# Optimization experiments

Measured on AMD Instinct MI355X. Metric: run time of the kernel, lower is better.

The kernel has to match this reference:

```python
import jax, jax.numpy as jnp
import numpy as np
from jax import lax

B, S, E = 8, 2048, 1024
NH, K = 4, 4
DH = E // NH  # 256


def setup_inputs() -> dict:
    key = jax.random.key(0)
    ks = jax.random.split(key, 8)
    sc = 0.02  # small_init-style scale
    return {
        "x": jax.random.normal(ks[0], (B, S, E), jnp.float32),
        "conv_w": jax.random.normal(ks[1], (K, 1, E), jnp.float32) * sc,  # depthwise (W,1,E)
        "conv_b": jnp.zeros((E,), jnp.float32),
        "fgate_w": jax.random.normal(ks[2], (NH, DH, DH), jnp.float32) * sc,
        "igate_w": jax.random.normal(ks[3], (NH, DH, DH), jnp.float32) * sc,
        "zgate_w": jax.random.normal(ks[4], (NH, DH, DH), jnp.float32) * sc,
        "ogate_w": jax.random.normal(ks[5], (NH, DH, DH), jnp.float32) * sc,
        "rkernel": jax.random.normal(ks[6], (NH, DH, 4 * DH), jnp.float32) * sc,
        "rbias": jnp.zeros((NH, 4, DH), jnp.float32),
        "gn_weight": jnp.ones((E,), jnp.float32),
    }


def _headwise(x, w):
    # LinearHeadwiseExpand, bias=False: einsum('...hd,hod->...ho')
    Bx, Sx, _ = x.shape
    return jnp.einsum('bshd,hod->bsho', x.reshape(Bx, Sx, NH, DH), w)


def reference(x, conv_w, conv_b, fgate_w, igate_w, zgate_w, ogate_w, rkernel, rbias, gn_weight):
    # --- causal depthwise conv1d + SiLU ---
    xp = jnp.pad(x, ((0, 0), (K - 1, 0), (0, 0)))  # left pad -> causal
    xc = lax.conv_general_dilated(
        xp, conv_w, window_strides=(1,), padding='VALID',
        dimension_numbers=('NWC', 'WIO', 'NWC'), feature_group_count=E) + conv_b
    x_conv = xc * jax.nn.sigmoid(xc)  # SiLU

    # --- headwise gate pre-activations (matches torch cat order [i,f,z,o]) ---
    gi = _headwise(x_conv, fgate_w)
    gf = _headwise(x_conv, igate_w)
    gz = _headwise(x, zgate_w)
    go = _headwise(x, ogate_w)
    gx = jnp.stack([gi, gf, gz, go], axis=3)      # (B,S,NH,4,DH)
    gx_t = jnp.moveaxis(gx, 1, 0)                 # (S,B,NH,4,DH)

    # --- stabilized exponential-gated sLSTM recurrence (xLSTM vanilla cell) ---
    z0 = jnp.zeros((B, NH, DH), x.dtype)

    def step(carry, xt):
        y, c, n, m = carry  # each (B,NH,DH)
        ry = jnp.einsum('bhd,hdk->bhk', y, rkernel).reshape(B, NH, 4, DH)
        raw = xt + ry + rbias
        ir, fr, zr, orr = raw[:, :, 0], raw[:, :, 1], raw[:, :, 2], raw[:, :, 3]
        logfplusm = m + jax.nn.log_sigmoid(fr)
        mnew = jnp.maximum(ir, logfplusm)
        ig = jnp.exp(ir - mnew)
        fg = jnp.exp(logfplusm - mnew)
        cnew = fg * c + ig * jnp.tanh(zr)
        nnew = fg * n + ig
        ynew = jax.nn.sigmoid(orr) * cnew / nnew
        return (ynew, cnew, nnew, mnew), ynew

    _, ys = lax.scan(step, (z0, z0, z0, z0), gx_t)  # ys: (S,B,NH,DH)
    y = jnp.moveaxis(ys, 0, 1)                       # (B,S,NH,DH)

    # --- MultiHeadLayerNorm: group_norm with num_groups=NH, weight only (no bias) ---
    mu = jnp.mean(y, axis=-1, keepdims=True)
    var = jnp.var(y, axis=-1, keepdims=True)
    yn = (y - mu) * lax.rsqrt(var + 1e-5)
    out = (yn * gn_weight.reshape(NH, DH)).reshape(B, S, E)
    return out
```

## Files before the change

kernel.cpp:

```cpp
#include <hip/hip_runtime.h>
#include <hip/hip_fp16.h>

#define BB 8
#define SS 2048
#define EE 1024
#define NHH 4
#define DHH 256

typedef _Float16 f16x2 __attribute__((ext_vector_type(2)));
typedef _Float16 f16x8 __attribute__((ext_vector_type(8)));
typedef float f32x4 __attribute__((ext_vector_type(4)));

__device__ __forceinline__ __half2 u2h2(unsigned int u) {
  union { unsigned int u; __half2 h; } c; c.u = u; return c.h;
}
__device__ __forceinline__ unsigned int h2u(__half2 h) {
  union { unsigned int u; __half2 h; } c; c.h = h; return c.u;
}

__global__ __launch_bounds__(256) void gates_gemm(
    const float* __restrict__ x, const float* __restrict__ conv_w,
    const float* __restrict__ conv_b,
    const float* __restrict__ fgw, const float* __restrict__ igw,
    const float* __restrict__ zgw, const float* __restrict__ ogw,
    __half* __restrict__ gx)
{
  __shared__ float Xs[8][11][33];
  __shared__ __half As[64][40];
  __shared__ __half Bs[64][40];

  const int tid = threadIdx.x;
  const int mt = blockIdx.x;
  const int nt = blockIdx.y;
  const int p  = blockIdx.z;
  const int h  = p >> 1, pair = p & 1;
  const int s0 = mt << 3;
  const int n0 = nt << 6;

  const float* W0 = pair ? zgw : fgw;
  const float* W1 = pair ? ogw : igw;

  const int w = tid >> 6, l = tid & 63;
  const int lrow = l & 15, kq = l >> 4;
  const int koff = kq << 3;

  f32x4 acc[4] = {};

  for (int d0 = 0; d0 < DHH; d0 += 32) {
    const int ebase = h * DHH + d0;

    if (pair == 0) {
      for (int i = tid; i < 8 * 11 * 32; i += 256) {
        int kk = i & 31, rest = i >> 5;
        int b = rest / 11, si = rest - b * 11;
        int sg = s0 - 3 + si;
        float v = 0.f;
        if (sg >= 0) v = x[((size_t)b * SS + sg) * EE + ebase + kk];
        Xs[b][si][kk] = v;
      }
      __syncthreads();
      for (int i = tid; i < 64 * 32; i += 256) {
        int kk = i & 31, r = i >> 5;
        int sl = r >> 3, b = r & 7;
        int e = ebase + kk;
        float xc = conv_b[e];
        xc = fmaf(Xs[b][sl + 0][kk], conv_w[0 * EE + e], xc);
        xc = fmaf(Xs[b][sl + 1][kk], conv_w[1 * EE + e], xc);
        xc = fmaf(Xs[b][sl + 2][kk], conv_w[2 * EE + e], xc);
        xc = fmaf(Xs[b][sl + 3][kk], conv_w[3 * EE + e], xc);
        float sg = 1.f / (1.f + __expf(-xc));
        As[r][kk] = __float2half(xc * sg);
      }
    } else {
      for (int i = tid; i < 64 * 32; i += 256) {
        int kk = i & 31, r = i >> 5;
        int sl = r >> 3, b = r & 7;
        As[r][kk] = __float2half(x[((size_t)b * SS + s0 + sl) * EE + ebase + kk]);
      }
    }
    for (int i = tid; i < 64 * 32; i += 256) {
      int k = i & 31, col = i >> 5;
      int o = n0 + col;
      const float* Wp = (o < 256) ? W0 : W1;
      int oo = o & 255;
      Bs[col][k] = __float2half(Wp[((size_t)h * DHH + oo) * DHH + d0 + k]);
    }
    __syncthreads();

    f16x8 bfrag = *(const f16x8*)&Bs[w * 16 + lrow][koff];
#pragma unroll
    for (int mtl = 0; mtl < 4; ++mtl) {
      f16x8 afrag = *(const f16x8*)&As[mtl * 16 + lrow][koff];
      acc[mtl] = __builtin_amdgcn_mfma_f32_16x16x32_f16(afrag, bfrag, acc[mtl], 0, 0, 0);
    }
    __syncthreads();
  }

#pragma unroll
  for (int mtl = 0; mtl < 4; ++mtl) {
#pragma unroll
    for (int j = 0; j < 4; ++j) {
      int row_loc = mtl * 16 + kq * 4 + j;
      int grow = s0 * 8 + row_loc;
      int colg = n0 + w * 16 + lrow;
      gx[(size_t)grow * 4096 + h * 1024 + pair * 512 + colg] = __float2half(acc[mtl][j]);
    }
  }
}

__global__ __launch_bounds__(512)
void slstm_scan4(
    const float* __restrict__ rk,
    const float* __restrict__ rb,
    const __half* __restrict__ gx,
    float* __restrict__ out)
{
  extern __shared__ unsigned char smem[];
  uint4* ldsB  = (uint4*)smem;
  __half* ypub = (__half*)(smem + 131072);
  float* rawb  = (float*)(smem + 132096);

  const int t = threadIdx.x;
  const int w = t >> 6, l = t & 63;
  const int lrow = l & 15, lkq = l >> 4;
  const int b = blockIdx.x >> 2, h = blockIdx.x & 3;
  const float* Rh = rk + (size_t)h * DHH * 1024;
  const int n0w = w << 7;

  f16x8 wB[6][8];
#pragma unroll
  for (int nt = 0; nt < 6; ++nt) {
    const int col = n0w + nt * 16 + lrow;
#pragma unroll
    for (int kt = 0; kt < 8; ++kt) {
      f16x8 f;
#pragma unroll
      for (int i = 0; i < 4; ++i) {
        const int k = kt * 32 + lkq * 8 + 2 * i;
        f[2 * i]     = (_Float16)Rh[(size_t)k * 1024 + col];
        f[2 * i + 1] = (_Float16)Rh[(size_t)(k + 1) * 1024 + col];
      }
      wB[nt][kt] = f;
    }
  }
  for (int j = 0; j < 2; ++j) {
    const int col = n0w + (6 + j) * 16 + lrow;
    for (int kt = 0; kt < 8; ++kt) {
      f16x8 f;
      for (int i = 0; i < 4; ++i) {
        const int k = kt * 32 + lkq * 8 + 2 * i;
        f[2 * i]     = (_Float16)Rh[(size_t)k * 1024 + col];
        f[2 * i + 1] = (_Float16)Rh[(size_t)(k + 1) * 1024 + col];
      }
      *(f16x8*)&ldsB[((w * 2 + j) * 8 + kt) * 64 + l] = f;
    }
  }

  const int d = t & 255;
  float rb0 = 0.f, rb1 = 0.f, rb2 = 0.f, rb3 = 0.f;
  if (t < 256) {
    rb0 = rb[h * 1024 + d];
    rb1 = rb[h * 1024 + 256 + d];
    rb2 = rb[h * 1024 + 512 + d];
    rb3 = rb[h * 1024 + 768 + d];
    ypub[d] = __float2half(0.f);
    ypub[256 + d] = __float2half(0.f);
  }
  __syncthreads();

  float cst = 0.f, nst = 0.f, mst = 0.f;
  const size_t gxstep = (size_t)BB * NHH * 1024;
  const __half* gp = gx + ((size_t)b * NHH + h) * 1024;
  float cx0 = 0.f, cx1 = 0.f, cx2 = 0.f, cx3 = 0.f;
  if (t < 256) {
    cx0 = __half2float(gp[d]);
    cx1 = __half2float(gp[256 + d]);
    cx2 = __half2float(gp[512 + d]);
    cx3 = __half2float(gp[768 + d]);
  }

  int cur = 0;
  for (int st = 0; st < SS; ++st) {
    __half nx0, nx1, nx2, nx3;
    if (t < 256) {
      const __half* pn = gp + (size_t)((st + 1 < SS) ? st + 1 : st) * gxstep;
      nx0 = pn[d]; nx1 = pn[256 + d]; nx2 = pn[512 + d]; nx3 = pn[768 + d];
    }

    const __half* yc = ypub + cur * 256;
    f32x4 a0 = {}, a1 = {}, a2 = {}, a3 = {}, a4 = {}, a5 = {}, a6 = {}, a7 = {};
#pragma unroll
    for (int kt = 0; kt < 8; ++kt) {
      f16x8 A = {};
      if (lrow == 0) A = *(const f16x8*)(yc + kt * 32 + lkq * 8);
      a0 = __builtin_amdgcn_mfma_f32_16x16x32_f16(A, wB[0][kt], a0, 0, 0, 0);
      a1 = __builtin_amdgcn_mfma_f32_16x16x32_f16(A, wB[1][kt], a1, 0, 0, 0);
      a2 = __builtin_amdgcn_mfma_f32_16x16x32_f16(A, wB[2][kt], a2, 0, 0, 0);
      a3 = __builtin_amdgcn_mfma_f32_16x16x32_f16(A, wB[3][kt], a3, 0, 0, 0);
      a4 = __builtin_amdgcn_mfma_f32_16x16x32_f16(A, wB[4][kt], a4, 0, 0, 0);
      a5 = __builtin_amdgcn_mfma_f32_16x16x32_f16(A, wB[5][kt], a5, 0, 0, 0);
      f16x8 b6 = *(const f16x8*)&ldsB[((w * 2 + 0) * 8 + kt) * 64 + l];
      f16x8 b7 = *(const f16x8*)&ldsB[((w * 2 + 1) * 8 + kt) * 64 + l];
      a6 = __builtin_amdgcn_mfma_f32_16x16x32_f16(A, b6, a6, 0, 0, 0);
      a7 = __builtin_amdgcn_mfma_f32_16x16x32_f16(A, b7, a7, 0, 0, 0);
    }
    if (l < 16) {
      rawb[n0w +   0 + l] = a0[0];
      rawb[n0w +  16 + l] = a1[0];
      rawb[n0w +  32 + l] = a2[0];
      rawb[n0w +  48 + l] = a3[0];
      rawb[n0w +  64 + l] = a4[0];
      rawb[n0w +  80 + l] = a5[0];
      rawb[n0w +  96 + l] = a6[0];
      rawb[n0w + 112 + l] = a7[0];
    }
    __syncthreads();

    if (t < 256) {
      float iv = rawb[d]       + cx0 + rb0;
      float fv = rawb[256 + d] + cx1 + rb1;
      float zv = rawb[512 + d] + cx2 + rb2;
      float ov = rawb[768 + d] + cx3 + rb3;

      float ea = __expf(-fabsf(fv));
      float ls = fminf(fv, 0.f) - __logf(1.f + ea);
      float lfm = mst + ls;
      float mn = fmaxf(iv, lfm);
      float ig = __expf(iv - mn);
      float fg = __expf(lfm - mn);
      float pz = __expf(-2.f * fabsf(zv));
      float tm = __fdividef(1.f - pz, 1.f + pz);
      float th = (zv < 0.f) ? -tm : tm;
      cst = fg * cst + ig * th;
      nst = fg * nst + ig;
      float og = __fdividef(1.f, 1.f + __expf(-ov));
      float y = og * __fdividef(cst, nst);
      mst = mn;

      out[((size_t)b * SS + st) * EE + h * DHH + d] = y;
      ypub[(cur ^ 1) * 256 + d] = __float2half(y);
    }
    __syncthreads();
    cur ^= 1;
    cx0 = __half2float(nx0); cx1 = __half2float(nx1);
    cx2 = __half2float(nx2); cx3 = __half2float(nx3);
  }
}

__global__ __launch_bounds__(256) void groupnorm(
    float* __restrict__ y, const float* __restrict__ gnw)
{
  const int row = blockIdx.x;
  const int t = threadIdx.x;
  float4 v = ((const float4*)y)[(size_t)row * 256 + t];
  float s = v.x + v.y + v.z + v.w;
  float q = v.x * v.x + v.y * v.y + v.z * v.z + v.w * v.w;
#pragma unroll
  for (int mask = 1; mask < 64; mask <<= 1) {
    s += __shfl_xor(s, mask, 64);
    q += __shfl_xor(q, mask, 64);
  }
  float mu = s * (1.f / 256.f);
  float var = q * (1.f / 256.f) - mu * mu;
  float rs = rsqrtf(var + 1e-5f);
  float4 g = ((const float4*)gnw)[t];
  float4 o;
  o.x = (v.x - mu) * rs * g.x;
  o.y = (v.y - mu) * rs * g.y;
  o.z = (v.z - mu) * rs * g.z;
  o.w = (v.w - mu) * rs * g.w;
  ((float4*)y)[(size_t)row * 256 + t] = o;
}

extern "C" void kernel_launch(void* const* d_in, const int* in_sizes, int n_in,
                              void* d_out, int out_size, void* d_ws, size_t ws_size,
                              hipStream_t stream) {
  const float* x      = (const float*)d_in[0];
  const float* conv_w = (const float*)d_in[1];
  const float* conv_b = (const float*)d_in[2];
  const float* fgw    = (const float*)d_in[3];
  const float* igw    = (const float*)d_in[4];
  const float* zgw    = (const float*)d_in[5];
  const float* ogw    = (const float*)d_in[6];
  const float* rk     = (const float*)d_in[7];
  const float* rb     = (const float*)d_in[8];
  const float* gnw    = (const float*)d_in[9];
  float* out = (float*)d_out;
  __half* gx = (__half*)d_ws;

  dim3 g1(256, 8, 8);
  gates_gemm<<<g1, 256, 0, stream>>>(x, conv_w, conv_b, fgw, igw, zgw, ogw, gx);

  const int scan_lds = 131072 + 1024 + 4096;
  (void)hipFuncSetAttribute(reinterpret_cast<const void*>(slstm_scan4),
                            hipFuncAttributeMaxDynamicSharedMemorySize, scan_lds);
  slstm_scan4<<<32, 512, scan_lds, stream>>>(rk, rb, gx, out);

  groupnorm<<<BB * SS, 256, 0, stream>>>(out, gnw);
}
```

Baseline: 4.348 ms.

## Keep more recurrent weights in registers and deepen gate prefetch in sLSTM scan

The scan kernel now holds 7 of 8 recurrent-weight column tiles per wave in registers instead of 6, which halves the LDS-resident weights and the per-step LDS reads. It preloads all A fragments and LDS B fragments before issuing the MFMAs, splits the MFMA chain into two groups of four accumulators, prefetches gate inputs two steps ahead instead of one, and replaces __syncthreads with an explicit lgkmcnt wait plus s_barrier. The aim is to shorten the serial per-timestep latency. The cost is higher register pressure, which risks spills. All lanes now load A instead of only lrow==0, which adds LDS traffic and may change results if the other rows were meant to be zero.

```diff
diff --git a/kernel.cpp b/kernel.cpp
--- a/kernel.cpp
+++ b/kernel.cpp
@@ -109,7 +109,7 @@
 }
 
 __global__ __launch_bounds__(512)
-void slstm_scan4(
+void slstm_scan5(
     const float* __restrict__ rk,
     const float* __restrict__ rb,
     const __half* __restrict__ gx,
@@ -117,8 +117,8 @@
 {
   extern __shared__ unsigned char smem[];
   uint4* ldsB  = (uint4*)smem;
-  __half* ypub = (__half*)(smem + 131072);
-  float* rawb  = (float*)(smem + 132096);
+  __half* ypub = (__half*)(smem + 65536);
+  float* rawb  = (float*)(smem + 66560);
 
   const int t = threadIdx.x;
   const int w = t >> 6, l = t & 63;
@@ -127,9 +127,9 @@
   const float* Rh = rk + (size_t)h * DHH * 1024;
   const int n0w = w << 7;
 
-  f16x8 wB[6][8];
-#pragma unroll
-  for (int nt = 0; nt < 6; ++nt) {
+  f16x8 wB[7][8];
+#pragma unroll
+  for (int nt = 0; nt < 7; ++nt) {
     const int col = n0w + nt * 16 + lrow;
 #pragma unroll
     for (int kt = 0; kt < 8; ++kt) {
@@ -143,8 +143,8 @@
       wB[nt][kt] = f;
     }
   }
-  for (int j = 0; j < 2; ++j) {
-    const int col = n0w + (6 + j) * 16 + lrow;
+  {
+    const int col = n0w + 112 + lrow;
     for (int kt = 0; kt < 8; ++kt) {
       f16x8 f;
       for (int i = 0; i < 4; ++i) {
@@ -152,7 +152,7 @@
         f[2 * i]     = (_Float16)Rh[(size_t)k * 1024 + col];
         f[2 * i + 1] = (_Float16)Rh[(size_t)(k + 1) * 1024 + col];
       }
-      *(f16x8*)&ldsB[((w * 2 + j) * 8 + kt) * 64 + l] = f;
+      *(f16x8*)&ldsB[(w * 8 + kt) * 64 + l] = f;
     }
   }
 
@@ -172,49 +172,70 @@
   const size_t gxstep = (size_t)BB * NHH * 1024;
   const __half* gp = gx + ((size_t)b * NHH + h) * 1024;
   float cx0 = 0.f, cx1 = 0.f, cx2 = 0.f, cx3 = 0.f;
+  __half nh0 = __float2half(0.f), nh1 = nh0, nh2 = nh0, nh3 = nh0;
   if (t < 256) {
     cx0 = __half2float(gp[d]);
     cx1 = __half2float(gp[256 + d]);
     cx2 = __half2float(gp[512 + d]);
     cx3 = __half2float(gp[768 + d]);
+    const __half* p1 = gp + gxstep;
+    nh0 = p1[d]; nh1 = p1[256 + d]; nh2 = p1[512 + d]; nh3 = p1[768 + d];
   }
 
   int cur = 0;
   for (int st = 0; st < SS; ++st) {
-    __half nx0, nx1, nx2, nx3;
+    __half p0 = nh0, p1 = nh1, p2 = nh2, p3 = nh3;
     if (t < 256) {
-      const __half* pn = gp + (size_t)((st + 1 < SS) ? st + 1 : st) * gxstep;
-      nx0 = pn[d]; nx1 = pn[256 + d]; nx2 = pn[512 + d]; nx3 = pn[768 + d];
+      const int sp = (st + 2 < SS) ? st + 2 : SS - 1;
+      const __half* pp = gp + (size_t)sp * gxstep;
+      p0 = pp[d]; p1 = pp[256 + d]; p2 = pp[512 + d]; p3 = pp[768 + d];
     }
 
     const __half* yc = ypub + cur * 256;
-    f32x4 a0 = {}, a1 = {}, a2 = {}, a3 = {}, a4 = {}, a5 = {}, a6 = {}, a7 = {};
-#pragma unroll
-    for (int kt = 0; kt < 8; ++kt) {
-      f16x8 A = {};
-      if (lrow == 0) A = *(const f16x8*)(yc + kt * 32 + lkq * 8);
-      a0 = __builtin_amdgcn_mfma_f32_16x16x32_f16(A, wB[0][kt], a0, 0, 0, 0);
-      a1 = __builtin_amdgcn_mfma_f32_16x16x32_f16(A, wB[1][kt], a1, 0, 0, 0);
-      a2 = __builtin_amdgcn_mfma_f32_16x16x32_f16(A, wB[2][kt], a2, 0, 0, 0);
-      a3 = __builtin_amdgcn_mfma_f32_16x16x32_f16(A, wB[3][kt], a3, 0, 0, 0);
-      a4 = __builtin_amdgcn_mfma_f32_16x16x32_f16(A, wB[4][kt], a4, 0, 0, 0);
-      a5 = __builtin_amdgcn_mfma_f32_16x16x32_f16(A, wB[5][kt], a5, 0, 0, 0);
-      f16x8 b6 = *(const f16x8*)&ldsB[((w * 2 + 0) * 8 + kt) * 64 + l];
-      f16x8 b7 = *(const f16x8*)&ldsB[((w * 2 + 1) * 8 + kt) * 64 + l];
-      a6 = __builtin_amdgcn_mfma_f32_16x16x32_f16(A, b6, a6, 0, 0, 0);
-      a7 = __builtin_amdgcn_mfma_f32_16x16x32_f16(A, b7, a7, 0, 0, 0);
-    }
-    if (l < 16) {
-      rawb[n0w +   0 + l] = a0[0];
-      rawb[n0w +  16 + l] = a1[0];
-      rawb[n0w +  32 + l] = a2[0];
-      rawb[n0w +  48 + l] = a3[0];
-      rawb[n0w +  64 + l] = a4[0];
-      rawb[n0w +  80 + l] = a5[0];
-      rawb[n0w +  96 + l] = a6[0];
-      rawb[n0w + 112 + l] = a7[0];
-    }
-    __syncthreads();
+    f16x8 Areg[8];
+#pragma unroll
+    for (int kt = 0; kt < 8; ++kt)
+      Areg[kt] = *(const f16x8*)(yc + kt * 32 + lkq * 8);
+    f16x8 b7[8];
+#pragma unroll
+    for (int kt = 0; kt < 8; ++kt)
+      b7[kt] = *(const f16x8*)&ldsB[(w * 8 + kt) * 64 + l];
+
+    {
+      f32x4 a0 = {}, a1 = {}, a2 = {}, a3 = {};
+#pragma unroll
+      for (int kt = 0; kt < 8; ++kt) {
+        a0 = __builtin_amdgcn_mfma_f32_16x16x32_f16(Areg[kt], wB[0][kt], a0, 0, 0, 0);
+        a1 = __builtin_amdgcn_mfma_f32_16x16x32_f16(Areg[kt], wB[1][kt], a1, 0, 0, 0);
+        a2 = __builtin_amdgcn_mfma_f32_16x16x32_f16(Areg[kt], wB[2][kt], a2, 0, 0, 0);
+        a3 = __builtin_amdgcn_mfma_f32_16x16x32_f16(Areg[kt], wB[3][kt], a3, 0, 0, 0);
+      }
+      if (l < 16) {
+        rawb[n0w +  0 + l] = a0[0];
+        rawb[n0w + 16 + l] = a1[0];
+        rawb[n0w + 32 + l] = a2[0];
+        rawb[n0w + 48 + l] = a3[0];
+      }
+    }
+    {
+      f32x4 c0 = {}, c1 = {}, c2 = {}, c3 = {};
+#pragma unroll
+      for (int kt = 0; kt < 8; ++kt) {
+        c0 = __builtin_amdgcn_mfma_f32_16x16x32_f16(Areg[kt], wB[4][kt], c0, 0, 0, 0);
+        c1 = __builtin_amdgcn_mfma_f32_16x16x32_f16(Areg[kt], wB[5][kt], c1, 0, 0, 0);
+        c2 = __builtin_amdgcn_mfma_f32_16x16x32_f16(Areg[kt], wB[6][kt], c2, 0, 0, 0);
+        c3 = __builtin_amdgcn_mfma_f32_16x16x32_f16(Areg[kt], b7[kt],    c3, 0, 0, 0);
+      }
+      if (l < 16) {
+        rawb[n0w +  64 + l] = c0[0];
+        rawb[n0w +  80 + l] = c1[0];
+        rawb[n0w +  96 + l] = c2[0];
+        rawb[n0w + 112 + l] = c3[0];
+      }
+    }
+
+    asm volatile("s_waitcnt lgkmcnt(0)" ::: "memory");
+    __builtin_amdgcn_s_barrier();
 
     if (t < 256) {
       float iv = rawb[d]       + cx0 + rb0;
@@ -240,10 +261,14 @@
       out[((size_t)b * SS + st) * EE + h * DHH + d] = y;
       ypub[(cur ^ 1) * 256 + d] = __float2half(y);
     }
-    __syncthreads();
+
+    asm volatile("s_waitcnt lgkmcnt(0)" ::: "memory");
+    __builtin_amdgcn_s_barrier();
+
     cur ^= 1;
-    cx0 = __half2float(nx0); cx1 = __half2float(nx1);
-    cx2 = __half2float(nx2); cx3 = __half2float(nx3);
+    cx0 = __half2float(nh0); cx1 = __half2float(nh1);
+    cx2 = __half2float(nh2); cx3 = __half2float(nh3);
+    nh0 = p0; nh1 = p1; nh2 = p2; nh3 = p3;
   }
 }
 
@@ -291,10 +316,10 @@
   dim3 g1(256, 8, 8);
   gates_gemm<<<g1, 256, 0, stream>>>(x, conv_w, conv_b, fgw, igw, zgw, ogw, gx);
 
-  const int scan_lds = 131072 + 1024 + 4096;
-  (void)hipFuncSetAttribute(reinterpret_cast<const void*>(slstm_scan4),
+  const int scan_lds = 65536 + 1024 + 4096;
+  (void)hipFuncSetAttribute(reinterpret_cast<const void*>(slstm_scan5),
                             hipFuncAttributeMaxDynamicSharedMemorySize, scan_lds);
-  slstm_scan4<<<32, 512, scan_lds, stream>>>(rk, rb, gx, out);
+  slstm_scan5<<<32, 512, scan_lds, stream>>>(rk, rb, gx, out);
 
   groupnorm<<<BB * SS, 256, 0, stream>>>(out, gnw);
 }
```

Result: slower. 11.17 ms (+156.8%).

## Split sLSTM recurrence across workgroups by hidden slice with global-memory flag exchange

Applied to the files above, without the earlier changes.

Instead of one workgroup per (batch, head) holding the whole recurrent matrix, each workgroup now owns a 32-column slice of the hidden dim for all 8 batches of one head. It keeps its weight slice entirely in registers and runs batched MFMA with 8 real rows instead of 1. Each step's y values are published to global memory with release flags and gathered from the 7 peer workgroups, which spin-wait on those flags. This trades LDS weight traffic and wasted MFMA rows for a per-step cross-workgroup synchronisation cost. It also relies on all 32 workgroups being co-resident, with a timeout fallback.

```diff
diff --git a/kernel.cpp b/kernel.cpp
--- a/kernel.cpp
+++ b/kernel.cpp
@@ -16,6 +16,9 @@
 }
 __device__ __forceinline__ unsigned int h2u(__half2 h) {
   union { unsigned int u; __half2 h; } c; c.h = h; return c.u;
+}
+__device__ __forceinline__ unsigned int packh2(float a, float b) {
+  return h2u(__floats2half2_rn(a, b));
 }
 
 __global__ __launch_bounds__(256) void gates_gemm(
@@ -109,118 +112,88 @@
 }
 
 __global__ __launch_bounds__(512)
-void slstm_scan4(
+void slstm_scan6(
     const float* __restrict__ rk,
     const float* __restrict__ rb,
     const __half* __restrict__ gx,
-    float* __restrict__ out)
+    float* __restrict__ out,
+    unsigned int* __restrict__ ybuf,
+    unsigned int* __restrict__ yflag)
 {
-  extern __shared__ unsigned char smem[];
-  uint4* ldsB  = (uint4*)smem;
-  __half* ypub = (__half*)(smem + 131072);
-  float* rawb  = (float*)(smem + 132096);
+  __shared__ __half ylds[8][272];
+  __shared__ float rawlds[4][32][8];
+  __shared__ int fw;
 
   const int t = threadIdx.x;
   const int w = t >> 6, l = t & 63;
   const int lrow = l & 15, lkq = l >> 4;
-  const int b = blockIdx.x >> 2, h = blockIdx.x & 3;
+  const int s = blockIdx.x >> 2, h = blockIdx.x & 3;
+  const int wg = s * 4 + h;
   const float* Rh = rk + (size_t)h * DHH * 1024;
-  const int n0w = w << 7;
-
-  f16x8 wB[6][8];
-#pragma unroll
-  for (int nt = 0; nt < 6; ++nt) {
-    const int col = n0w + nt * 16 + lrow;
+
+  const int gw = w >> 1, hw = w & 1;
+  const int colg = gw * 256 + s * 32 + hw * 16 + lrow;
+
+  f16x8 wB[8];
+#pragma unroll
+  for (int kt = 0; kt < 8; ++kt) {
+    f16x8 f;
+#pragma unroll
+    for (int i = 0; i < 8; ++i) {
+      const int k = kt * 32 + lkq * 8 + i;
+      f[i] = (_Float16)Rh[(size_t)k * 1024 + colg];
+    }
+    wB[kt] = f;
+  }
+
+  const int dloc = (t >> 3) & 31, bs = t & 7;
+  const int dglob = s * 32 + dloc;
+  float rbv[4] = {};
+  if (t < 256) {
+#pragma unroll
+    for (int g = 0; g < 4; ++g) rbv[g] = rb[h * 1024 + g * 256 + dglob];
+  }
+
+  for (int i = t; i < 8 * 272; i += 512) ((__half*)ylds)[i] = __float2half(0.f);
+  if (t == 0) fw = 0;
+  __syncthreads();
+
+  const size_t gxstep = (size_t)BB * NHH * 1024;
+  const __half* gpz = gx + ((size_t)bs * NHH + h) * 1024;
+  float cx[4] = {};
+  __half nh[4] = {};
+  if (t < 256) {
+#pragma unroll
+    for (int g = 0; g < 4; ++g) cx[g] = __half2float(gpz[g * 256 + dglob]);
+  }
+
+  float cst = 0.f, nstt = 0.f, mst = 0.f;
+
+  for (int st = 0; st < SS; ++st) {
+    const int slot = st & 3;
+    if (t < 256) {
+      const int sp = (st + 1 < SS) ? st + 1 : st;
+#pragma unroll
+      for (int g = 0; g < 4; ++g) nh[g] = gpz[(size_t)sp * gxstep + g * 256 + dglob];
+    }
+
+    f32x4 acc = {};
 #pragma unroll
     for (int kt = 0; kt < 8; ++kt) {
-      f16x8 f;
-#pragma unroll
-      for (int i = 0; i < 4; ++i) {
-        const int k = kt * 32 + lkq * 8 + 2 * i;
-        f[2 * i]     = (_Float16)Rh[(size_t)k * 1024 + col];
-        f[2 * i + 1] = (_Float16)Rh[(size_t)(k + 1) * 1024 + col];
-      }
-      wB[nt][kt] = f;
-    }
-  }
-  for (int j = 0; j < 2; ++j) {
-    const int col = n0w + (6 + j) * 16 + lrow;
-    for (int kt = 0; kt < 8; ++kt) {
-      f16x8 f;
-      for (int i = 0; i < 4; ++i) {
-        const int k = kt * 32 + lkq * 8 + 2 * i;
-        f[2 * i]     = (_Float16)Rh[(size_t)k * 1024 + col];
-        f[2 * i + 1] = (_Float16)Rh[(size_t)(k + 1) * 1024 + col];
-      }
-      *(f16x8*)&ldsB[((w * 2 + j) * 8 + kt) * 64 + l] = f;
-    }
-  }
-
-  const int d = t & 255;
-  float rb0 = 0.f, rb1 = 0.f, rb2 = 0.f, rb3 = 0.f;
-  if (t < 256) {
-    rb0 = rb[h * 1024 + d];
-    rb1 = rb[h * 1024 + 256 + d];
-    rb2 = rb[h * 1024 + 512 + d];
-    rb3 = rb[h * 1024 + 768 + d];
-    ypub[d] = __float2half(0.f);
-    ypub[256 + d] = __float2half(0.f);
-  }
-  __syncthreads();
-
-  float cst = 0.f, nst = 0.f, mst = 0.f;
-  const size_t gxstep = (size_t)BB * NHH * 1024;
-  const __half* gp = gx + ((size_t)b * NHH + h) * 1024;
-  float cx0 = 0.f, cx1 = 0.f, cx2 = 0.f, cx3 = 0.f;
-  if (t < 256) {
-    cx0 = __half2float(gp[d]);
-    cx1 = __half2float(gp[256 + d]);
-    cx2 = __half2float(gp[512 + d]);
-    cx3 = __half2float(gp[768 + d]);
-  }
-
-  int cur = 0;
-  for (int st = 0; st < SS; ++st) {
-    __half nx0, nx1, nx2, nx3;
+      f16x8 A = *(const f16x8*)&ylds[lrow & 7][kt * 32 + lkq * 8];
+      acc = __builtin_amdgcn_mfma_f32_16x16x32_f16(A, wB[kt], acc, 0, 0, 0);
+    }
+    if (l < 32) {
+      *(f32x4*)&rawlds[gw][hw * 16 + lrow][lkq * 4] = acc;
+    }
+    __syncthreads();
+
+    float y = 0.f;
     if (t < 256) {
-      const __half* pn = gp + (size_t)((st + 1 < SS) ? st + 1 : st) * gxstep;
-      nx0 = pn[d]; nx1 = pn[256 + d]; nx2 = pn[512 + d]; nx3 = pn[768 + d];
-    }
-
-    const __half* yc = ypub + cur * 256;
-    f32x4 a0 = {}, a1 = {}, a2 = {}, a3 = {}, a4 = {}, a5 = {}, a6 = {}, a7 = {};
-#pragma unroll
-    for (int kt = 0; kt < 8; ++kt) {
-      f16x8 A = {};
-      if (lrow == 0) A = *(const f16x8*)(yc + kt * 32 + lkq * 8);
-      a0 = __builtin_amdgcn_mfma_f32_16x16x32_f16(A, wB[0][kt], a0, 0, 0, 0);
-      a1 = __builtin_amdgcn_mfma_f32_16x16x32_f16(A, wB[1][kt], a1, 0, 0, 0);
-      a2 = __builtin_amdgcn_mfma_f32_16x16x32_f16(A, wB[2][kt], a2, 0, 0, 0);
-      a3 = __builtin_amdgcn_mfma_f32_16x16x32_f16(A, wB[3][kt], a3, 0, 0, 0);
-      a4 = __builtin_amdgcn_mfma_f32_16x16x32_f16(A, wB[4][kt], a4, 0, 0, 0);
-      a5 = __builtin_amdgcn_mfma_f32_16x16x32_f16(A, wB[5][kt], a5, 0, 0, 0);
-      f16x8 b6 = *(const f16x8*)&ldsB[((w * 2 + 0) * 8 + kt) * 64 + l];
-      f16x8 b7 = *(const f16x8*)&ldsB[((w * 2 + 1) * 8 + kt) * 64 + l];
-      a6 = __builtin_amdgcn_mfma_f32_16x16x32_f16(A, b6, a6, 0, 0, 0);
-      a7 = __builtin_amdgcn_mfma_f32_16x16x32_f16(A, b7, a7, 0, 0, 0);
-    }
-    if (l < 16) {
-      rawb[n0w +   0 + l] = a0[0];
-      rawb[n0w +  16 + l] = a1[0];
-      rawb[n0w +  32 + l] = a2[0];
-      rawb[n0w +  48 + l] = a3[0];
-      rawb[n0w +  64 + l] = a4[0];
-      rawb[n0w +  80 + l] = a5[0];
-      rawb[n0w +  96 + l] = a6[0];
-      rawb[n0w + 112 + l] = a7[0];
-    }
-    __syncthreads();
-
-    if (t < 256) {
-      float iv = rawb[d]       + cx0 + rb0;
-      float fv = rawb[256 + d] + cx1 + rb1;
-      float zv = rawb[512 + d] + cx2 + rb2;
-      float ov = rawb[768 + d] + cx3 + rb3;
+      float iv = rawlds[0][dloc][bs] + cx[0] + rbv[0];
+      float fv = rawlds[1][dloc][bs] + cx[1] + rbv[1];
+      float zv = rawlds[2][dloc][bs] + cx[2] + rbv[2];
+      float ov = rawlds[3][dloc][bs] + cx[3] + rbv[3];
 
       float ea = __expf(-fabsf(fv));
       float ls = fminf(fv, 0.f) - __logf(1.f + ea);
@@ -232,18 +205,53 @@
       float tm = __fdividef(1.f - pz, 1.f + pz);
       float th = (zv < 0.f) ? -tm : tm;
       cst = fg * cst + ig * th;
-      nst = fg * nst + ig;
+      nstt = fg * nstt + ig;
       float og = __fdividef(1.f, 1.f + __expf(-ov));
-      float y = og * __fdividef(cst, nst);
+      y = og * __fdividef(cst, nstt);
       mst = mn;
-
-      out[((size_t)b * SS + st) * EE + h * DHH + d] = y;
-      ypub[(cur ^ 1) * 256 + d] = __float2half(y);
-    }
-    __syncthreads();
-    cur ^= 1;
-    cx0 = __half2float(nx0); cx1 = __half2float(nx1);
-    cx2 = __half2float(nx2); cx3 = __half2float(nx3);
+      ylds[bs][dglob] = __float2half(y);
+    }
+    float ypart = __shfl_down(y, 1);
+    if (t < 256 && (bs & 1) == 0) {
+      unsigned int u = packh2(y, ypart);
+      int i = dloc * 4 + (bs >> 1);
+      __hip_atomic_store(&ybuf[wg * 512 + slot * 128 + i], u,
+                         __ATOMIC_RELAXED, __HIP_MEMORY_SCOPE_AGENT);
+    }
+    __syncthreads();
+    if (t == 0)
+      __hip_atomic_store(&yflag[wg * 4 + slot], (unsigned)(st + 1),
+                         __ATOMIC_RELEASE, __HIP_MEMORY_SCOPE_AGENT);
+    if (t < 256)
+      out[((size_t)bs * SS + st) * EE + h * DHH + dglob] = y;
+
+    if (w >= 1 && l == 0 && fw == 0) {
+      const int ps = (w - 1 < s) ? (w - 1) : w;
+      const unsigned want = (unsigned)(st + 1);
+      int it = 0;
+      while (__hip_atomic_load(&yflag[(ps * 4 + h) * 4 + slot],
+                               __ATOMIC_ACQUIRE, __HIP_MEMORY_SCOPE_AGENT) < want) {
+        __builtin_amdgcn_s_sleep(1);
+        if (++it > (1 << 20)) { fw = 1; break; }
+      }
+    }
+    __syncthreads();
+    __threadfence();
+
+    for (int idx = t; idx < 7 * 128; idx += 512) {
+      const int p = idx >> 7;
+      const int ps = (p < s) ? p : p + 1;
+      const int i = idx & 127;
+      unsigned int u = __hip_atomic_load(&ybuf[(ps * 4 + h) * 512 + slot * 128 + i],
+                                         __ATOMIC_RELAXED, __HIP_MEMORY_SCOPE_AGENT);
+      __half2 hh = u2h2(u);
+      const int dl = i >> 2, b0 = (i & 3) * 2;
+      ylds[b0][ps * 32 + dl]     = __low2half(hh);
+      ylds[b0 + 1][ps * 32 + dl] = __high2half(hh);
+    }
+    __syncthreads();
+#pragma unroll
+    for (int g = 0; g < 4; ++g) cx[g] = __half2float(nh[g]);
   }
 }
 
@@ -286,15 +294,17 @@
   const float* rb     = (const float*)d_in[8];
   const float* gnw    = (const float*)d_in[9];
   float* out = (float*)d_out;
+
   __half* gx = (__half*)d_ws;
+  unsigned int* ybuf  = (unsigned int*)((char*)d_ws + 134217728);
+  unsigned int* yflag = (unsigned int*)((char*)d_ws + 134217728 + 65536);
+
+  (void)hipMemsetAsync(ybuf, 0, 65536 + 512, stream);
 
   dim3 g1(256, 8, 8);
   gates_gemm<<<g1, 256, 0, stream>>>(x, conv_w, conv_b, fgw, igw, zgw, ogw, gx);
 
-  const int scan_lds = 131072 + 1024 + 4096;
-  (void)hipFuncSetAttribute(reinterpret_cast<const void*>(slstm_scan4),
-                            hipFuncAttributeMaxDynamicSharedMemorySize, scan_lds);
-  slstm_scan4<<<32, 512, scan_lds, stream>>>(rk, rb, gx, out);
+  slstm_scan6<<<32, 512, 0, stream>>>(rk, rb, gx, out, ybuf, yflag);
 
   groupnorm<<<BB * SS, 256, 0, stream>>>(out, gnw);
 }
```

Measured after the change: 17.36 ms. 299% more time.
